# Kernel optimization log

Hardware: AMD Instinct MI355X
Metric: run time of the kernel (lower is better)

The kernel has to match this reference:

```python
import jax, jax.numpy as jnp
import numpy as np

N = 100000
E = 1600000
F_IN = 32
H = 64
EDGE_DIM = 2
OUT = 1
NEG_SLOPE = 0.2


def setup_inputs() -> dict:
    key = jax.random.key(0)
    ks = jax.random.split(key, 20)
    g = lambda k, shape, fan_in: jax.random.normal(k, shape, jnp.float32) / np.sqrt(fan_in)
    inp = {
        "x": jax.random.normal(ks[0], (N, F_IN), jnp.float32),
        "edge_index": jax.random.randint(ks[1], (2, E), 0, N, jnp.int32),
        "edge_attr": jax.random.normal(ks[2], (E, EDGE_DIM), jnp.float32),
        # GATConv layer 1 (in=F_IN, out=H, heads=1, edge_dim=EDGE_DIM)
        "W1": g(ks[3], (F_IN, H), F_IN),
        "as1": g(ks[4], (H,), H),
        "ad1": g(ks[5], (H,), H),
        "We1": g(ks[6], (EDGE_DIM, H), EDGE_DIM),
        "ae1": g(ks[7], (H,), H),
        "b1": jnp.zeros((H,), jnp.float32),
        # GATConv layer 2 (in=H, out=H)
        "W2": g(ks[8], (H, H), H),
        "as2": g(ks[9], (H,), H),
        "ad2": g(ks[10], (H,), H),
        "We2": g(ks[11], (EDGE_DIM, H), EDGE_DIM),
        "ae2": g(ks[12], (H,), H),
        "b2": jnp.zeros((H,), jnp.float32),
        # Linear head
        "Wl": g(ks[13], (H, OUT), H),
        "bl": jnp.zeros((OUT,), jnp.float32),
    }
    return inp


def gat_conv(x, src, dst, edge_attr, W, att_src, att_dst, We, att_e, bias):
    """PyG GATConv, heads=1, add_self_loops=True (fill_value='mean'), eval mode."""
    n = x.shape[0]
    # add self-loops; self-loop edge_attr = mean of edge_attr (fill_value='mean')
    loop_attr = jnp.mean(edge_attr, axis=0)
    src_a = jnp.concatenate([src, jnp.arange(n, dtype=src.dtype)])
    dst_a = jnp.concatenate([dst, jnp.arange(n, dtype=dst.dtype)])
    ea = jnp.concatenate([edge_attr, jnp.broadcast_to(loop_attr, (n, edge_attr.shape[1]))])
    h = x @ W                          # [n, H]
    a_src = h @ att_src                # [n]
    a_dst = h @ att_dst                # [n]
    a_edge = (ea @ We) @ att_e         # [E+n]
    alpha = a_src[src_a] + a_dst[dst_a] + a_edge
    alpha = jax.nn.leaky_relu(alpha, NEG_SLOPE)
    # segment softmax over incoming edges of each destination node
    amax = jax.ops.segment_max(alpha, dst_a, num_segments=n)
    ex = jnp.exp(alpha - amax[dst_a])
    denom = jax.ops.segment_sum(ex, dst_a, num_segments=n)
    w = ex / denom[dst_a]              # every node has a self-loop -> denom > 0
    out = jax.ops.segment_sum(h[src_a] * w[:, None], dst_a, num_segments=n)
    return out + bias


def reference(x, edge_index, edge_attr, W1, as1, ad1, We1, ae1, b1,
              W2, as2, ad2, We2, ae2, b2, Wl, bl):
    src, dst = edge_index[0], edge_index[1]
    h = gat_conv(x, src, dst, edge_attr, W1, as1, ad1, We1, ae1, b1)
    h = jax.nn.relu(h)  # dropout is identity in eval mode
    h = gat_conv(h, src, dst, edge_attr, W2, as2, ad2, We2, ae2, b2)
    h = h @ Wl + bl
    return jax.nn.relu(h)
```

## Files before the change

### kernel.cpp

```cpp
#include <hip/hip_runtime.h>
#include <hip/hip_fp16.h>
#include <cstdint>

#define HH 64
#define NEG 0.2f
#define NB 1024
#define SH 7
#define BKCAP 1024
#define ECAP 4096

__device__ __forceinline__ float leaky(float x){ return x > 0.f ? x : NEG * x; }

__global__ void k_hist(const int* __restrict__ dst, const float* __restrict__ ea,
                       int* __restrict__ ghist, float2* __restrict__ pbuf,
                       int E, int nbkt, int CH){
    __shared__ int hist[BKCAP];
    __shared__ float2 sm[4];
    for (int i = threadIdx.x; i < nbkt; i += 256) hist[i] = 0;
    __syncthreads();
    int b = blockIdx.x;
    int e0 = b * CH, e1 = min(E, e0 + CH);
    float s0 = 0.f, s1 = 0.f;
    for (int e = e0 + threadIdx.x; e < e1; e += 256){
        int d = dst[e];
        atomicAdd(&hist[d >> SH], 1);
        float2 v = *reinterpret_cast<const float2*>(ea + 2ll * e);
        s0 += v.x; s1 += v.y;
    }
    #pragma unroll
    for (int o = 32; o; o >>= 1){ s0 += __shfl_xor(s0, o); s1 += __shfl_xor(s1, o); }
    int wv = threadIdx.x >> 6;
    if ((threadIdx.x & 63) == 0) sm[wv] = make_float2(s0, s1);
    __syncthreads();
    if (threadIdx.x == 0){
        float2 a = sm[0], c = sm[1], d2 = sm[2], f = sm[3];
        pbuf[b] = make_float2(a.x + c.x + d2.x + f.x, a.y + c.y + d2.y + f.y);
    }
    for (int i = threadIdx.x; i < nbkt; i += 256)
        ghist[(size_t)b * nbkt + i] = hist[i];
}

__global__ void k_const(const float* __restrict__ We1, const float* __restrict__ ae1,
                        const float* __restrict__ We2, const float* __restrict__ ae2,
                        const float2* __restrict__ pbuf, float* __restrict__ cbuf,
                        float invE, int nbp){
    int k = threadIdx.x;
    float m0 = 0.f, m1 = 0.f;
    for (int i = k; i < nbp; i += 64){ float2 u = pbuf[i]; m0 += u.x; m1 += u.y; }
    float p0 = We1[k] * ae1[k], p1 = We1[64 + k] * ae1[k];
    float q0 = We2[k] * ae2[k], q1 = We2[64 + k] * ae2[k];
    #pragma unroll
    for (int o = 32; o; o >>= 1){
        m0 += __shfl_xor(m0, o); m1 += __shfl_xor(m1, o);
        p0 += __shfl_xor(p0, o); p1 += __shfl_xor(p1, o);
        q0 += __shfl_xor(q0, o); q1 += __shfl_xor(q1, o);
    }
    if (k == 0){
        m0 *= invE; m1 *= invE;
        cbuf[4] = p0; cbuf[5] = p1; cbuf[6] = q0; cbuf[7] = q1;
        cbuf[2] = m0 * p0 + m1 * p1;
        cbuf[3] = m0 * q0 + m1 * q1;
    }
}

__global__ void k_scanA(const int* __restrict__ ghist, int* __restrict__ incl,
                        int* __restrict__ part, int M, int nbkt){
    __shared__ int sm[256];
    int tid = threadIdx.x;
    int i = blockIdx.x * 256 + tid;
    int v = 0;
    if (i < M) v = ghist[(size_t)(i % NB) * nbkt + (i / NB)];
    int x = v;
    sm[tid] = x; __syncthreads();
    for (int o = 1; o < 256; o <<= 1){
        int t = (tid >= o) ? sm[tid - o] : 0;
        __syncthreads();
        x += t; sm[tid] = x;
        __syncthreads();
    }
    if (i < M) incl[i] = x;
    if (tid == 255) part[blockIdx.x] = x;
}

__global__ void k_scanB(int* __restrict__ part, int nb){
    __shared__ int sm[1024];
    int tid = threadIdx.x;
    int C = (nb + 1023) >> 10;
    if (C > 8) C = 8;
    int base = tid * C;
    int vals[8];
    int s = 0;
    #pragma unroll
    for (int k = 0; k < 8; ++k){
        if (k < C){
            int i = base + k;
            int v = (i < nb) ? part[i] : 0;
            vals[k] = v; s += v;
        }
    }
    sm[tid] = s; __syncthreads();
    int x = s;
    for (int o = 1; o < 1024; o <<= 1){
        int t = (tid >= o) ? sm[tid - o] : 0;
        __syncthreads();
        x += t; sm[tid] = x;
        __syncthreads();
    }
    int excl = x - s;
    #pragma unroll
    for (int k = 0; k < 8; ++k){
        if (k < C){
            int i = base + k;
            if (i < nb){ int v = vals[k]; part[i] = excl; excl += v; }
        }
    }
}

__global__ void k_scanC(const int* __restrict__ ghist, const int* __restrict__ incl,
                        const int* __restrict__ part, int* __restrict__ gbase,
                        int M, int nbkt){
    int i = blockIdx.x * 256 + threadIdx.x;
    if (i < M){
        int v = ghist[(size_t)(i % NB) * nbkt + (i / NB)];
        gbase[i] = part[blockIdx.x] + incl[i] - v;
    }
}

__global__ void k_scatter(const int* __restrict__ src, const int* __restrict__ dst,
                          const float* __restrict__ ea, const int* __restrict__ gbase,
                          const float* __restrict__ cbuf, uint2* __restrict__ csort,
                          int E, int nbkt, int CH){
    __shared__ int cur[BKCAP];
    int b = blockIdx.x;
    for (int i = threadIdx.x; i < nbkt; i += 256) cur[i] = gbase[(size_t)i * NB + b];
    __syncthreads();
    float c4 = cbuf[4], c5 = cbuf[5], c6 = cbuf[6], c7 = cbuf[7];
    int e0 = b * CH, e1 = min(E, e0 + CH);
    for (int e = e0 + threadIdx.x; e < e1; e += 256){
        int d = dst[e];
        float2 v = *reinterpret_cast<const float2*>(ea + 2ll * e);
        float a1 = v.x * c4 + v.y * c5;
        float a2 = v.x * c6 + v.y * c7;
        __half2 ah = __floats2half2_rn(a1, a2);
        int p = atomicAdd(&cur[d >> SH], 1);
        uint2 o;
        o.x = (unsigned)src[e] | ((unsigned)(d & ((1 << SH) - 1)) << 20);
        o.y = *reinterpret_cast<unsigned*>(&ah);
        csort[p] = o;
    }
}

__global__ void __launch_bounds__(256, 1) k_bucket(
        const uint2* __restrict__ csort, const int* __restrict__ gbase,
        uint2* __restrict__ rec, int* __restrict__ row_ptr,
        int E, int n, int nbkt){
    __shared__ uint2 lrec[ECAP];
    __shared__ uint2 srec[ECAP];
    __shared__ int nhist[128], ncur[128], sscan[128];
    int tid = threadIdx.x;
    int bkt = blockIdx.x;
    int base = gbase[(size_t)bkt * NB];
    int end  = (bkt + 1 < nbkt) ? gbase[(size_t)(bkt + 1) * NB] : E;
    int cnt = min(end - base, ECAP);
    if (tid < 128) nhist[tid] = 0;
    __syncthreads();
    for (int j = tid; j < cnt; j += 256){
        uint2 r = csort[base + j];
        lrec[j] = r;
        atomicAdd(&nhist[(r.x >> 20) & 127], 1);
    }
    __syncthreads();
    int v = (tid < 128) ? nhist[tid] : 0;
    if (tid < 128) sscan[tid] = v;
    __syncthreads();
    for (int o = 1; o < 128; o <<= 1){
        int t = 0;
        if (tid < 128 && tid >= o) t = sscan[tid - o];
        __syncthreads();
        if (tid < 128) sscan[tid] += t;
        __syncthreads();
    }
    if (tid < 128){
        int st = sscan[tid] - v;
        ncur[tid] = st;
        int node = (bkt << SH) + tid;
        if (node < n) row_ptr[node] = base + st;
    }
    if (bkt == 0 && tid == 255) row_ptr[n] = E;
    __syncthreads();
    for (int j = tid; j < cnt; j += 256){
        uint2 r = lrec[j];
        int dl = (r.x >> 20) & 127;
        int p = atomicAdd(&ncur[dl], 1);
        srec[p] = make_uint2(r.x & 0xFFFFFu, r.y);
    }
    __syncthreads();
    for (int j = tid; j < cnt; j += 256)
        rec[base + j] = srec[j];
}

template<int F, bool HALFIN>
__global__ void k_feat(const void* __restrict__ inp, const float* __restrict__ W,
                       const float* __restrict__ as_, const float* __restrict__ ad_,
                       __half* __restrict__ h, float* __restrict__ asrc,
                       float* __restrict__ adst, int n){
    int lane = threadIdx.x & 63;
    int wid0 = (blockIdx.x * blockDim.x + threadIdx.x) >> 6;
    int nw   = (gridDim.x * blockDim.x) >> 6;
    float wcol[F];
    #pragma unroll
    for (int i = 0; i < F; ++i) wcol[i] = W[i * HH + lane];
    float asl = as_[lane], adl = ad_[lane];
    for (int wid = wid0; wid < n; wid += nw){
        int u = __builtin_amdgcn_readfirstlane(wid);
        float a0 = 0.f, a1 = 0.f, a2 = 0.f, a3 = 0.f;
        if constexpr (!HALFIN){
            const float* __restrict__ row = (const float*)inp + (size_t)u * F;
            #pragma unroll
            for (int i = 0; i < F; i += 4){
                a0 += row[i]     * wcol[i];
                a1 += row[i + 1] * wcol[i + 1];
                a2 += row[i + 2] * wcol[i + 2];
                a3 += row[i + 3] * wcol[i + 3];
            }
        } else {
            const unsigned* __restrict__ row =
                (const unsigned*)((const __half*)inp + (size_t)u * F);
            #pragma unroll
            for (int i = 0; i < F / 2; i += 2){
                unsigned p0 = row[i], p1 = row[i + 1];
                __half2 h0 = *reinterpret_cast<__half2*>(&p0);
                __half2 h1 = *reinterpret_cast<__half2*>(&p1);
                float2 f0 = __half22float2(h0), f1 = __half22float2(h1);
                a0 += f0.x * wcol[2 * i];
                a1 += f0.y * wcol[2 * i + 1];
                a2 += f1.x * wcol[2 * i + 2];
                a3 += f1.y * wcol[2 * i + 3];
            }
        }
        float acc = (a0 + a1) + (a2 + a3);
        h[(size_t)u * HH + lane] = __float2half(acc);
        float vs = acc * asl, vd = acc * adl;
        #pragma unroll
        for (int o = 32; o; o >>= 1){ vs += __shfl_xor(vs, o); vd += __shfl_xor(vd, o); }
        if (lane == 0){ asrc[u] = vs; adst[u] = vd; }
    }
}

template<int AFIELD, bool RELU, bool HEAD>
__global__ void k_fused(const __half* __restrict__ h, const uint2* __restrict__ rec,
                        const int* __restrict__ row_ptr, const float* __restrict__ asrc,
                        const float* __restrict__ adst, const float* __restrict__ cbuf,
                        const float* __restrict__ bias, const float* __restrict__ Wl,
                        const float* __restrict__ bl, __half* __restrict__ outh,
                        float* __restrict__ outf, int n){
    int tid  = blockIdx.x * blockDim.x + threadIdx.x;
    int wave = tid >> 6;
    int lane = threadIdx.x & 63;
    int grp  = lane >> 3;
    int l7   = lane & 7;
    int node = wave * 8 + grp;
    bool valid = node < n;
    int nc = valid ? node : 0;
    int b  = row_ptr[nc];
    int e2 = valid ? row_ptr[nc + 1] : b;
    float ad = adst[nc];
    float aself = leaky(asrc[nc] + ad + cbuf[AFIELD == 1 ? 2 : 3]);
    float exs = __expf(aself);
    float dsum = exs;
    float acc[8];
    {
        float4 q = *reinterpret_cast<const float4*>(h + (size_t)nc * HH + (l7 << 3));
        const __half2* ph = reinterpret_cast<const __half2*>(&q);
        #pragma unroll
        for (int i = 0; i < 4; ++i){
            float2 f = __half22float2(ph[i]);
            acc[2 * i]     = exs * f.x;
            acc[2 * i + 1] = exs * f.y;
        }
    }
    auto pick = [](uint2 rr) -> float {
        __half2 ah = *reinterpret_cast<const __half2*>(&rr.y);
        return (AFIELD == 1) ? __low2float(ah) : __high2float(ah);
    };
    int j = b;
    for (; j + 3 < e2; j += 4){
        uint2 r0 = rec[j], r1 = rec[j + 1], r2 = rec[j + 2], r3 = rec[j + 3];
        int s0 = (int)r0.x, s1 = (int)r1.x, s2 = (int)r2.x, s3 = (int)r3.x;
        float w0 = __expf(leaky(asrc[s0] + ad + pick(r0)));
        float w1 = __expf(leaky(asrc[s1] + ad + pick(r1)));
        float w2 = __expf(leaky(asrc[s2] + ad + pick(r2)));
        float w3 = __expf(leaky(asrc[s3] + ad + pick(r3)));
        dsum += (w0 + w1) + (w2 + w3);
        float4 q0 = *reinterpret_cast<const float4*>(h + (size_t)s0 * HH + (l7 << 3));
        float4 q1 = *reinterpret_cast<const float4*>(h + (size_t)s1 * HH + (l7 << 3));
        float4 q2 = *reinterpret_cast<const float4*>(h + (size_t)s2 * HH + (l7 << 3));
        float4 q3 = *reinterpret_cast<const float4*>(h + (size_t)s3 * HH + (l7 << 3));
        const __half2* p0 = reinterpret_cast<const __half2*>(&q0);
        const __half2* p1 = reinterpret_cast<const __half2*>(&q1);
        const __half2* p2 = reinterpret_cast<const __half2*>(&q2);
        const __half2* p3 = reinterpret_cast<const __half2*>(&q3);
        #pragma unroll
        for (int i = 0; i < 4; ++i){
            float2 f0 = __half22float2(p0[i]);
            float2 f1 = __half22float2(p1[i]);
            float2 f2 = __half22float2(p2[i]);
            float2 f3 = __half22float2(p3[i]);
            acc[2 * i]     += w0 * f0.x + w1 * f1.x + w2 * f2.x + w3 * f3.x;
            acc[2 * i + 1] += w0 * f0.y + w1 * f1.y + w2 * f2.y + w3 * f3.y;
        }
    }
    for (; j < e2; ++j){
        uint2 rr = rec[j];
        int s = (int)rr.x;
        float w = __expf(leaky(asrc[s] + ad + pick(rr)));
        dsum += w;
        float4 q = *reinterpret_cast<const float4*>(h + (size_t)s * HH + (l7 << 3));
        const __half2* ph = reinterpret_cast<const __half2*>(&q);
        #pragma unroll
        for (int i = 0; i < 4; ++i){
            float2 f = __half22float2(ph[i]);
            acc[2 * i]     += w * f.x;
            acc[2 * i + 1] += w * f.y;
        }
    }
    float inv = 1.f / dsum;
    float4 b0 = *reinterpret_cast<const float4*>(bias + (l7 << 3));
    float4 b1 = *reinterpret_cast<const float4*>(bias + (l7 << 3) + 4);
    float r[8];
    r[0] = acc[0] * inv + b0.x; r[1] = acc[1] * inv + b0.y;
    r[2] = acc[2] * inv + b0.z; r[3] = acc[3] * inv + b0.w;
    r[4] = acc[4] * inv + b1.x; r[5] = acc[5] * inv + b1.y;
    r[6] = acc[6] * inv + b1.z; r[7] = acc[7] * inv + b1.w;
    if (RELU){
        #pragma unroll
        for (int i = 0; i < 8; ++i) r[i] = fmaxf(r[i], 0.f);
    }
    if (!HEAD){
        if (valid){
            __half2 q01 = __floats2half2_rn(r[0], r[1]);
            __half2 q23 = __floats2half2_rn(r[2], r[3]);
            __half2 q45 = __floats2half2_rn(r[4], r[5]);
            __half2 q67 = __floats2half2_rn(r[6], r[7]);
            uint4 st;
            st.x = *reinterpret_cast<unsigned*>(&q01);
            st.y = *reinterpret_cast<unsigned*>(&q23);
            st.z = *reinterpret_cast<unsigned*>(&q45);
            st.w = *reinterpret_cast<unsigned*>(&q67);
            *reinterpret_cast<uint4*>(outh + (size_t)node * HH + (l7 << 3)) = st;
        }
    } else {
        float4 w0 = *reinterpret_cast<const float4*>(Wl + (l7 << 3));
        float4 w1 = *reinterpret_cast<const float4*>(Wl + (l7 << 3) + 4);
        float v = r[0] * w0.x + r[1] * w0.y + r[2] * w0.z + r[3] * w0.w
                + r[4] * w1.x + r[5] * w1.y + r[6] * w1.z + r[7] * w1.w;
        v += __shfl_xor(v, 1); v += __shfl_xor(v, 2); v += __shfl_xor(v, 4);
        if (valid && l7 == 0) outf[node] = fmaxf(v + bl[0], 0.f);
    }
}

extern "C" void kernel_launch(void* const* d_in, const int* in_sizes, int n_in,
                              void* d_out, int out_size, void* d_ws, size_t ws_size,
                              hipStream_t stream) {
    const float* x   = (const float*)d_in[0];
    const int*   ei  = (const int*)  d_in[1];
    const float* ea  = (const float*)d_in[2];
    const float* W1  = (const float*)d_in[3];
    const float* as1 = (const float*)d_in[4];
    const float* ad1 = (const float*)d_in[5];
    const float* We1 = (const float*)d_in[6];
    const float* ae1 = (const float*)d_in[7];
    const float* b1  = (const float*)d_in[8];
    const float* W2  = (const float*)d_in[9];
    const float* as2 = (const float*)d_in[10];
    const float* ad2 = (const float*)d_in[11];
    const float* We2 = (const float*)d_in[12];
    const float* ae2 = (const float*)d_in[13];
    const float* b2  = (const float*)d_in[14];
    const float* Wl  = (const float*)d_in[15];
    const float* bl  = (const float*)d_in[16];
    float* out = (float*)d_out;

    const int N = in_sizes[0] / 32;
    const int E = in_sizes[1] / 2;
    const int* srcI = ei;
    const int* dstI = ei + E;

    const int nbkt = (N + (1 << SH) - 1) >> SH;
    const int M    = nbkt * NB;
    const int CH   = (E + NB - 1) / NB;
    const int gMs  = (M + 255) / 256;

    char* ws = (char*)d_ws;
    size_t off = 0;
    auto alloc = [&](size_t bytes)->char*{
        char* p = ws + off;
        off += (bytes + 255) & ~size_t(255);
        return p;
    };
    __half*  hbuf   = (__half*) alloc((size_t)N * HH * 2);
    __half*  bufB   = (__half*) alloc((size_t)N * HH * 2);
    uint2*   rec    = (uint2*)  alloc((size_t)E * 8);
    uint2*   csort  = (uint2*)  alloc((size_t)E * 8);
    int*     ghist  = (int*)    alloc((size_t)M * 4);
    int*     incl   = (int*)    alloc((size_t)M * 4);
    int*     gbase  = (int*)    alloc((size_t)M * 4);
    int*     part   = (int*)    alloc((size_t)gMs * 4);
    int*     row_ptr= (int*)    alloc((size_t)(N + 1) * 4);
    float*   asrc   = (float*)  alloc((size_t)N * 4);
    float*   adst   = (float*)  alloc((size_t)N * 4);
    float2*  pbuf   = (float2*) alloc((size_t)NB * 8);
    float*   cbuf   = (float*)  alloc(64);
    if (off > ws_size) return;

    const int BLK = 256;
    int gF = ((size_t)N * 8 + BLK - 1) / BLK;

    hipMemsetAsync(cbuf, 0, 64, stream);

    k_hist<<<NB, BLK, 0, stream>>>(dstI, ea, ghist, pbuf, E, nbkt, CH);
    k_const<<<1, 64, 0, stream>>>(We1, ae1, We2, ae2, pbuf, cbuf, 1.f / (float)E, NB);
    k_scanA<<<gMs, 256, 0, stream>>>(ghist, incl, part, M, nbkt);
    k_scanB<<<1, 1024, 0, stream>>>(part, gMs);
    k_scanC<<<gMs, 256, 0, stream>>>(ghist, incl, part, gbase, M, nbkt);
    k_scatter<<<NB, BLK, 0, stream>>>(srcI, dstI, ea, gbase, cbuf, csort, E, nbkt, CH);
    k_bucket<<<nbkt, BLK, 0, stream>>>(csort, gbase, rec, row_ptr, E, N, nbkt);

    k_feat<32, false><<<2048, BLK, 0, stream>>>(x, W1, as1, ad1, hbuf, asrc, adst, N);
    k_fused<1, true, false><<<gF, BLK, 0, stream>>>(hbuf, rec, row_ptr, asrc, adst,
                                                    cbuf, b1, nullptr, nullptr, bufB, nullptr, N);

    k_feat<64, true><<<2048, BLK, 0, stream>>>(bufB, W2, as2, ad2, hbuf, asrc, adst, N);
    k_fused<2, false, true><<<gF, BLK, 0, stream>>>(hbuf, rec, row_ptr, asrc, adst,
                                                    cbuf, b2, Wl, bl, nullptr, out, N);
}
```

Before: 201.5 us.

## Stage scatter records in LDS per chunk and write coalesced bucket runs

```diff
diff --git a/kernel.cpp b/kernel.cpp
--- a/kernel.cpp
+++ b/kernel.cpp
@@ -4,10 +4,11 @@
 
 #define HH 64
 #define NEG 0.2f
-#define NB 1024
+#define NB 256
 #define SH 7
 #define BKCAP 1024
 #define ECAP 4096
+#define CHCAP 6272
 
 __device__ __forceinline__ float leaky(float x){ return x > 0.f ? x : NEG * x; }
 
@@ -15,13 +16,13 @@
                        int* __restrict__ ghist, float2* __restrict__ pbuf,
                        int E, int nbkt, int CH){
     __shared__ int hist[BKCAP];
-    __shared__ float2 sm[4];
-    for (int i = threadIdx.x; i < nbkt; i += 256) hist[i] = 0;
+    __shared__ float2 sm[8];
+    for (int i = threadIdx.x; i < nbkt; i += 512) hist[i] = 0;
     __syncthreads();
     int b = blockIdx.x;
     int e0 = b * CH, e1 = min(E, e0 + CH);
     float s0 = 0.f, s1 = 0.f;
-    for (int e = e0 + threadIdx.x; e < e1; e += 256){
+    for (int e = e0 + threadIdx.x; e < e1; e += 512){
         int d = dst[e];
         atomicAdd(&hist[d >> SH], 1);
         float2 v = *reinterpret_cast<const float2*>(ea + 2ll * e);
@@ -33,10 +34,12 @@
     if ((threadIdx.x & 63) == 0) sm[wv] = make_float2(s0, s1);
     __syncthreads();
     if (threadIdx.x == 0){
-        float2 a = sm[0], c = sm[1], d2 = sm[2], f = sm[3];
-        pbuf[b] = make_float2(a.x + c.x + d2.x + f.x, a.y + c.y + d2.y + f.y);
-    }
-    for (int i = threadIdx.x; i < nbkt; i += 256)
+        float m0 = 0.f, m1 = 0.f;
+        #pragma unroll
+        for (int i = 0; i < 8; ++i){ m0 += sm[i].x; m1 += sm[i].y; }
+        pbuf[b] = make_float2(m0, m1);
+    }
+    for (int i = threadIdx.x; i < nbkt; i += 512)
         ghist[(size_t)b * nbkt + i] = hist[i];
 }
 
@@ -126,28 +129,57 @@
     }
 }
 
-__global__ void k_scatter(const int* __restrict__ src, const int* __restrict__ dst,
-                          const float* __restrict__ ea, const int* __restrict__ gbase,
-                          const float* __restrict__ cbuf, uint2* __restrict__ csort,
-                          int E, int nbkt, int CH){
+__global__ void k_scatter2(const int* __restrict__ src, const int* __restrict__ dst,
+                           const float* __restrict__ ea, const int* __restrict__ ghist,
+                           const int* __restrict__ gbase, const float* __restrict__ cbuf,
+                           uint2* __restrict__ csort, int E, int nbkt, int CH){
+    __shared__ uint2 srec[CHCAP];
+    __shared__ unsigned short bktof[CHCAP];
+    __shared__ int gb[BKCAP];
     __shared__ int cur[BKCAP];
+    __shared__ int wsum[512];
+    int tid = threadIdx.x;
     int b = blockIdx.x;
-    for (int i = threadIdx.x; i < nbkt; i += 256) cur[i] = gbase[(size_t)i * NB + b];
+    int base2 = tid * 2;
+    int v0 = 0, v1 = 0;
+    if (base2 < nbkt)     v0 = ghist[(size_t)b * nbkt + base2];
+    if (base2 + 1 < nbkt) v1 = ghist[(size_t)b * nbkt + base2 + 1];
+    int s = v0 + v1;
+    wsum[tid] = s; __syncthreads();
+    int x = s;
+    for (int o = 1; o < 512; o <<= 1){
+        int t = (tid >= o) ? wsum[tid - o] : 0;
+        __syncthreads();
+        x += t; wsum[tid] = x;
+        __syncthreads();
+    }
+    int excl = x - s;
+    if (base2 < nbkt)     cur[base2]     = excl;
+    if (base2 + 1 < nbkt) cur[base2 + 1] = excl + v0;
+    __syncthreads();
+    for (int i = tid; i < nbkt; i += 512)
+        gb[i] = gbase[(size_t)i * NB + b] - cur[i];
     __syncthreads();
     float c4 = cbuf[4], c5 = cbuf[5], c6 = cbuf[6], c7 = cbuf[7];
     int e0 = b * CH, e1 = min(E, e0 + CH);
-    for (int e = e0 + threadIdx.x; e < e1; e += 256){
+    for (int e = e0 + tid; e < e1; e += 512){
         int d = dst[e];
+        int bkt = d >> SH;
         float2 v = *reinterpret_cast<const float2*>(ea + 2ll * e);
         float a1 = v.x * c4 + v.y * c5;
         float a2 = v.x * c6 + v.y * c7;
         __half2 ah = __floats2half2_rn(a1, a2);
-        int p = atomicAdd(&cur[d >> SH], 1);
+        int p = atomicAdd(&cur[bkt], 1);
         uint2 o;
         o.x = (unsigned)src[e] | ((unsigned)(d & ((1 << SH) - 1)) << 20);
         o.y = *reinterpret_cast<unsigned*>(&ah);
-        csort[p] = o;
-    }
+        srec[p] = o;
+        bktof[p] = (unsigned short)bkt;
+    }
+    __syncthreads();
+    int cnt = e1 - e0;
+    for (int j = tid; j < cnt; j += 512)
+        csort[gb[bktof[j]] + j] = srec[j];
 }
 
 __global__ void __launch_bounds__(256, 1) k_bucket(
@@ -416,14 +448,12 @@
     const int BLK = 256;
     int gF = ((size_t)N * 8 + BLK - 1) / BLK;
 
-    hipMemsetAsync(cbuf, 0, 64, stream);
-
-    k_hist<<<NB, BLK, 0, stream>>>(dstI, ea, ghist, pbuf, E, nbkt, CH);
+    k_hist<<<NB, 512, 0, stream>>>(dstI, ea, ghist, pbuf, E, nbkt, CH);
     k_const<<<1, 64, 0, stream>>>(We1, ae1, We2, ae2, pbuf, cbuf, 1.f / (float)E, NB);
     k_scanA<<<gMs, 256, 0, stream>>>(ghist, incl, part, M, nbkt);
     k_scanB<<<1, 1024, 0, stream>>>(part, gMs);
     k_scanC<<<gMs, 256, 0, stream>>>(ghist, incl, part, gbase, M, nbkt);
-    k_scatter<<<NB, BLK, 0, stream>>>(srcI, dstI, ea, gbase, cbuf, csort, E, nbkt, CH);
+    k_scatter2<<<NB, 512, 0, stream>>>(srcI, dstI, ea, ghist, gbase, cbuf, csort, E, nbkt, CH);
     k_bucket<<<nbkt, BLK, 0, stream>>>(csort, gbase, rec, row_ptr, E, N, nbkt);
 
     k_feat<32, false><<<2048, BLK, 0, stream>>>(x, W1, as1, ad1, hbuf, asrc, adst, N);
```

Result: faster. 177.8 us (-11.7%).
